# Kernel optimization log

Measured on AMD Instinct MI355X. Metric: run time of the kernel, lower is better.

## Reference

```python
import jax, jax.numpy as jnp
import numpy as np

BS, T = 128, 256
N_AGENTS, STATE_DIM, EMBED_DIM, HYPERNET_EMBED = 32, 512, 64, 256


def setup_inputs() -> dict:
    key = jax.random.key(0)
    ks = jax.random.split(key, 16)
    s = 0.02  # param init scale
    return {
        "agent_qs": jax.random.normal(ks[0], (BS, T, N_AGENTS), jnp.float32),
        "states": jax.random.normal(ks[1], (BS, T, STATE_DIM), jnp.float32),
        "w1_0": jax.random.normal(ks[2], (HYPERNET_EMBED, STATE_DIM), jnp.float32) * s,
        "b1_0": jax.random.normal(ks[3], (HYPERNET_EMBED,), jnp.float32) * s,
        "w1_2": jax.random.normal(ks[4], (EMBED_DIM * N_AGENTS, HYPERNET_EMBED), jnp.float32) * s,
        "b1_2": jax.random.normal(ks[5], (EMBED_DIM * N_AGENTS,), jnp.float32) * s,
        "wf_0": jax.random.normal(ks[6], (HYPERNET_EMBED, STATE_DIM), jnp.float32) * s,
        "bf_0": jax.random.normal(ks[7], (HYPERNET_EMBED,), jnp.float32) * s,
        "wf_2": jax.random.normal(ks[8], (EMBED_DIM, HYPERNET_EMBED), jnp.float32) * s,
        "bf_2": jax.random.normal(ks[9], (EMBED_DIM,), jnp.float32) * s,
        "hb_w": jax.random.normal(ks[10], (EMBED_DIM, STATE_DIM), jnp.float32) * s,
        "hb_b": jax.random.normal(ks[11], (EMBED_DIM,), jnp.float32) * s,
        "v0_w": jax.random.normal(ks[12], (EMBED_DIM, STATE_DIM), jnp.float32) * s,
        "v0_b": jax.random.normal(ks[13], (EMBED_DIM,), jnp.float32) * s,
        "v2_w": jax.random.normal(ks[14], (1, EMBED_DIM), jnp.float32) * s,
        "v2_b": jax.random.normal(ks[15], (1,), jnp.float32) * s,
    }


def reference(agent_qs, states, w1_0, b1_0, w1_2, b1_2, wf_0, bf_0, wf_2, bf_2,
              hb_w, hb_b, v0_w, v0_b, v2_w, v2_b):
    bs = agent_qs.shape[0]
    s = states.reshape(-1, STATE_DIM)          # [B, S]
    q = agent_qs.reshape(-1, 1, N_AGENTS)       # [B, 1, A]
    # hypernet-generated first-layer weights (positive via abs)
    h1 = jax.nn.relu(s @ w1_0.T + b1_0)
    w1 = jnp.abs(h1 @ w1_2.T + b1_2).reshape(-1, N_AGENTS, EMBED_DIM)  # [B, A, E]
    b1 = (s @ hb_w.T + hb_b).reshape(-1, 1, EMBED_DIM)                 # [B, 1, E]
    hidden = jax.nn.elu(jnp.einsum('bia,bae->bie', q, w1) + b1)        # [B, 1, E]
    # hypernet-generated final weights
    hf = jax.nn.relu(s @ wf_0.T + bf_0)
    w_final = jnp.abs(hf @ wf_2.T + bf_2).reshape(-1, EMBED_DIM, 1)    # [B, E, 1]
    v = (jax.nn.relu(s @ v0_w.T + v0_b) @ v2_w.T + v2_b).reshape(-1, 1, 1)
    y = jnp.einsum('bie,beo->bio', hidden, w_final) + v                # [B, 1, 1]
    return y.reshape(bs, -1, 1)
```

## Files before the change

kernel.cpp:

```cpp
#include <hip/hip_runtime.h>


#define SDIM 512
#define HD   256
#define EDIM 64
#define NAG  32

typedef short short8v __attribute__((ext_vector_type(8)));
typedef short short4v __attribute__((ext_vector_type(4)));
typedef float f32x4  __attribute__((ext_vector_type(4)));

__device__ __forceinline__ unsigned short f2bf(float f) {
  unsigned int u = __float_as_uint(f);
  unsigned int r = (u + 0x7FFFu + ((u >> 16) & 1u)) >> 16;
  return (unsigned short)r;
}

__device__ __forceinline__ short4v cvt4(float4 a) {
  short4v r;
  r[0] = (short)f2bf(a.x); r[1] = (short)f2bf(a.y);
  r[2] = (short)f2bf(a.z); r[3] = (short)f2bf(a.w);
  return r;
}

__global__ void qmix_convert(const float* __restrict__ w1_0, const float* __restrict__ wf_0,
                             const float* __restrict__ hb_w, const float* __restrict__ v0_w,
                             const float* __restrict__ w1_2, const float* __restrict__ wf_2,
                             unsigned short* __restrict__ W0cat, unsigned short* __restrict__ w12b,
                             unsigned short* __restrict__ wf2b) {
  int i = blockIdx.x * 256 + threadIdx.x;
  if (i < 327680) {
    float v;
    if (i < 131072)      v = w1_0[i];
    else if (i < 262144) v = wf_0[i - 131072];
    else if (i < 294912) v = hb_w[i - 262144];
    else                 v = v0_w[i - 294912];
    W0cat[i] = f2bf(v);
  } else if (i < 851968) {
    w12b[i - 327680] = f2bf(w1_2[i - 327680]);
  } else if (i < 868352) {
    wf2b[i - 851968] = f2bf(wf_2[i - 851968]);
  }
}

__global__ __launch_bounds__(512, 2) void qmix_main(
    const float* __restrict__ agent_qs, const float* __restrict__ states,
    const unsigned short* __restrict__ W0cat, const unsigned short* __restrict__ w12b,
    const unsigned short* __restrict__ wf2b,
    const float* __restrict__ b1_0, const float* __restrict__ bf_0,
    const float* __restrict__ hb_b, const float* __restrict__ v0_b,
    const float* __restrict__ v2_w, const float* __restrict__ b1_2,
    const float* __restrict__ bf_2, const float* __restrict__ v2_b,
    float* __restrict__ out)
{
  __shared__ unsigned short sA[64 * 512];
  __shared__ unsigned short bb[2][16384];
  __shared__ float b1t[64 * 65];
  __shared__ float q_lds[64 * 33];
  __shared__ float vrow[64];
  __shared__ float ypart[2][64];

  const int t    = threadIdx.x;
  const int r0   = blockIdx.x * 64;
  const int wave = t >> 6, lane = t & 63;
  const int lrow = lane & 15, lk = lane >> 4;

  const float4* gS4 = (const float4*)(states + (size_t)r0 * SDIM);
  float4 L[16];
#pragma unroll
  for (int it = 0; it < 16; it++) L[it] = gS4[it * 512 + t];
  float4 qreg = ((const float4*)(agent_qs + (size_t)r0 * NAG))[t];

  const int colbase = wave * 80;
  const unsigned short* bp[5];
#pragma unroll
  for (int f = 0; f < 5; f++)
    bp[f] = W0cat + (size_t)(colbase + f * 16 + lrow) * SDIM + 8 * lk;
  short8v bregs[2][5];
#pragma unroll
  for (int f = 0; f < 5; f++) bregs[0][f] = *(const short8v*)(bp[f]);
#pragma unroll
  for (int f = 0; f < 5; f++) bregs[1][f] = *(const short8v*)(bp[f] + 32);

#pragma unroll
  for (int it = 0; it < 16; it++) {
    int idx = it * 512 + t;
    int row = idx >> 7, c4 = idx & 127;
    int byte = (row * 1024 + c4 * 8) ^ ((row & 7) << 4);
    *(short4v*)((char*)sA + byte) = cvt4(L[it]);
  }
  {
    int qrow = t >> 3, qc = (t & 7) * 4;
    q_lds[qrow * 33 + qc + 0] = qreg.x;
    q_lds[qrow * 33 + qc + 1] = qreg.y;
    q_lds[qrow * 33 + qc + 2] = qreg.z;
    q_lds[qrow * 33 + qc + 3] = qreg.w;
  }
  __syncthreads();

  f32x4 acc[4][5];
#pragma unroll
  for (int i = 0; i < 4; i++)
#pragma unroll
    for (int f = 0; f < 5; f++) acc[i][f] = (f32x4){0.f, 0.f, 0.f, 0.f};

#pragma unroll
  for (int ks = 0; ks < 16; ks++) {
    const int p = ks & 1;
    short8v af[4];
#pragma unroll
    for (int i = 0; i < 4; i++) {
      int row = i * 16 + lrow;
      int byte = (row * 1024 + ks * 64 + lk * 16) ^ ((row & 7) << 4);
      af[i] = *(const short8v*)((const char*)sA + byte);
    }
#pragma unroll
    for (int f = 0; f < 5; f++)
#pragma unroll
      for (int i = 0; i < 4; i++)
        acc[i][f] = __builtin_amdgcn_mfma_f32_16x16x32_bf16(af[i], bregs[p][f], acc[i][f], 0, 0, 0);
    if (ks < 14) {
#pragma unroll
      for (int f = 0; f < 5; f++) bregs[p][f] = *(const short8v*)(bp[f] + (ks + 2) * 32);
    }
  }

  __syncthreads();

  {
    float vs[4][4];
#pragma unroll
    for (int i = 0; i < 4; i++)
#pragma unroll
      for (int rr = 0; rr < 4; rr++) vs[i][rr] = 0.f;

#pragma unroll
    for (int f = 0; f < 5; f++) {
      int cb  = colbase + f * 16;
      int col = cb + lrow;
      if (cb < 512) {
        float bv = (cb < 256) ? b1_0[col] : bf_0[col - 256];
#pragma unroll
        for (int i = 0; i < 4; i++)
#pragma unroll
          for (int rr = 0; rr < 4; rr++) {
            int row = i * 16 + lk * 4 + rr;
            float v = fmaxf(acc[i][f][rr] + bv, 0.f);
            int byte = (row * 1024 + col * 2) ^ ((row & 7) << 4);
            *(unsigned short*)((char*)sA + byte) = f2bf(v);
          }
      } else if (cb < 576) {
        int e = col - 512;
        float bv = hb_b[e];
#pragma unroll
        for (int i = 0; i < 4; i++)
#pragma unroll
          for (int rr = 0; rr < 4; rr++) {
            int row = i * 16 + lk * 4 + rr;
            b1t[row * 65 + e] = acc[i][f][rr] + bv;
          }
      } else {
        int e = col - 576;
        float bv = v0_b[e], wv = v2_w[e];
#pragma unroll
        for (int i = 0; i < 4; i++)
#pragma unroll
          for (int rr = 0; rr < 4; rr++)
            vs[i][rr] = fmaf(fmaxf(acc[i][f][rr] + bv, 0.f), wv, vs[i][rr]);
      }
    }
    if (colbase == 560) {
#pragma unroll
      for (int i = 0; i < 4; i++)
#pragma unroll
        for (int rr = 0; rr < 4; rr++) {
          float v = vs[i][rr];
#pragma unroll
          for (int m = 1; m < 16; m <<= 1) v += __shfl_xor(v, m, 64);
          if (lrow == 0) vrow[i * 16 + lk * 4 + rr] = v;
        }
    }
  }

  short8v sreg[4];
#pragma unroll
  for (int rd = 0; rd < 4; rd++)
    sreg[rd] = *(const short8v*)(w12b + rd * 4096 + t * 8);

  __syncthreads();

  const int wr = wave >> 1;
  const int wc = wave & 1;

  short8v afr[8];
  {
    int row = wr * 16 + lrow;
#pragma unroll
    for (int kf = 0; kf < 8; kf++) {
      int byte = (row * 1024 + kf * 64 + lk * 16) ^ ((row & 7) << 4);
      afr[kf] = *(const short8v*)((const char*)sA + byte);
    }
  }

#pragma unroll
  for (int rd = 0; rd < 4; rd++) {
    int Lo = rd * 8192 + t * 16;
    int byte = Lo ^ (((Lo >> 9) & 7) << 4);
    *(short8v*)((char*)bb + byte) = sreg[rd];
  }
  __syncthreads();

  f32x4 hac[2];
  hac[0] = (f32x4){0.f, 0.f, 0.f, 0.f};
  hac[1] = (f32x4){0.f, 0.f, 0.f, 0.f};

#pragma unroll 1
  for (int a = 0; a < NAG; a++) {
    if (a < NAG - 1) {
      const unsigned short* src = w12b + (size_t)(a + 1) * 16384;
#pragma unroll
      for (int rd = 0; rd < 4; rd++)
        sreg[rd] = *(const short8v*)(src + rd * 4096 + t * 8);
    }
    const char* rbase = (const char*)bb + (a & 1) * 32768;

    f32x4 T[2];
    T[0] = (f32x4){0.f, 0.f, 0.f, 0.f};
    T[1] = (f32x4){0.f, 0.f, 0.f, 0.f};
#pragma unroll
    for (int kf = 0; kf < 8; kf++) {
      short8v bfv[2];
#pragma unroll
      for (int j = 0; j < 2; j++) {
        int e = wc * 32 + j * 16 + lrow;
        int Lo = e * 512 + kf * 64 + lk * 16;
        bfv[j] = *(const short8v*)(rbase + (Lo ^ ((e & 7) << 4)));
      }
#pragma unroll
      for (int j = 0; j < 2; j++)
        T[j] = __builtin_amdgcn_mfma_f32_16x16x32_bf16(afr[kf], bfv[j], T[j], 0, 0, 0);
    }

    float bbias[2];
#pragma unroll
    for (int j = 0; j < 2; j++) bbias[j] = b1_2[a * 64 + wc * 32 + j * 16 + lrow];
    float qv[4];
#pragma unroll
    for (int r = 0; r < 4; r++)
      qv[r] = q_lds[(wr * 16 + lk * 4 + r) * 33 + a];
#pragma unroll
    for (int j = 0; j < 2; j++)
#pragma unroll
      for (int r = 0; r < 4; r++)
        hac[j][r] = fmaf(qv[r], fabsf(T[j][r] + bbias[j]), hac[j][r]);

    if (a < NAG - 1) {
      char* wbase = (char*)bb + ((a & 1) ^ 1) * 32768;
#pragma unroll
      for (int rd = 0; rd < 4; rd++) {
        int Lo = rd * 8192 + t * 16;
        *(short8v*)(wbase + (Lo ^ (((Lo >> 9) & 7) << 4))) = sreg[rd];
      }
    }
    __syncthreads();
  }

  f32x4 wfa[2];
  wfa[0] = (f32x4){0.f, 0.f, 0.f, 0.f};
  wfa[1] = (f32x4){0.f, 0.f, 0.f, 0.f};
  {
    int row = wr * 16 + lrow;
#pragma unroll
    for (int kf = 0; kf < 8; kf++) {
      int byte = (row * 1024 + 512 + kf * 64 + lk * 16) ^ ((row & 7) << 4);
      short8v af2 = *(const short8v*)((const char*)sA + byte);
      short8v bf2v[2];
#pragma unroll
      for (int j = 0; j < 2; j++) {
        int e = wc * 32 + j * 16 + lrow;
        bf2v[j] = *(const short8v*)(wf2b + (size_t)e * HD + kf * 32 + 8 * lk);
      }
#pragma unroll
      for (int j = 0; j < 2; j++)
        wfa[j] = __builtin_amdgcn_mfma_f32_16x16x32_bf16(af2, bf2v[j], wfa[j], 0, 0, 0);
    }
  }

  {
    float ys[4];
#pragma unroll
    for (int r = 0; r < 4; r++) ys[r] = 0.f;
#pragma unroll
    for (int r = 0; r < 4; r++) {
      int row = wr * 16 + lk * 4 + r;
#pragma unroll
      for (int j = 0; j < 2; j++) {
        int e = wc * 32 + j * 16 + lrow;
        float pre = hac[j][r] + b1t[row * 65 + e];
        float h = pre > 0.f ? pre : expm1f(pre);
        float wfv = fabsf(wfa[j][r] + bf_2[e]);
        ys[r] = fmaf(h, wfv, ys[r]);
      }
    }
#pragma unroll
    for (int m = 1; m < 16; m <<= 1)
#pragma unroll
      for (int r = 0; r < 4; r++) ys[r] += __shfl_xor(ys[r], m, 64);
    if (lrow == 0) {
#pragma unroll
      for (int r = 0; r < 4; r++)
        ypart[wc][wr * 16 + lk * 4 + r] = ys[r];
    }
  }
  __syncthreads();
  if (t < 64) {
    out[r0 + t] = ypart[0][t] + ypart[1][t] + vrow[t] + v2_b[0];
  }
}

extern "C" void kernel_launch(void* const* d_in, const int* in_sizes, int n_in,
                              void* d_out, int out_size, void* d_ws, size_t ws_size,
                              hipStream_t stream) {
  const float* agent_qs = (const float*)d_in[0];
  const float* states   = (const float*)d_in[1];
  const float* w1_0 = (const float*)d_in[2];
  const float* b1_0 = (const float*)d_in[3];
  const float* w1_2 = (const float*)d_in[4];
  const float* b1_2 = (const float*)d_in[5];
  const float* wf_0 = (const float*)d_in[6];
  const float* bf_0 = (const float*)d_in[7];
  const float* wf_2 = (const float*)d_in[8];
  const float* bf_2 = (const float*)d_in[9];
  const float* hb_w = (const float*)d_in[10];
  const float* hb_b = (const float*)d_in[11];
  const float* v0_w = (const float*)d_in[12];
  const float* v0_b = (const float*)d_in[13];
  const float* v2_w = (const float*)d_in[14];
  const float* v2_b = (const float*)d_in[15];

  char* ws = (char*)d_ws;
  unsigned short* W0cat = (unsigned short*)ws;
  unsigned short* w12b  = (unsigned short*)(ws + 655360);
  unsigned short* wf2b  = (unsigned short*)(ws + 1703936);

  qmix_convert<<<3392, 256, 0, stream>>>(w1_0, wf_0, hb_w, v0_w, w1_2, wf_2,
                                         W0cat, w12b, wf2b);
  qmix_main<<<512, 512, 0, stream>>>(agent_qs, states, W0cat, w12b, wf2b,
                                     b1_0, bf_0, hb_b, v0_b, v2_w, b1_2, bf_2, v2_b,
                                     (float*)d_out);
}
```

Before: 124.8 us.

## Split agent loop across wave groups, load w1_2 fragments directly into registers

The 32-agent hypernet loop no longer stages w1_2 tiles through double-buffered LDS with a block-wide barrier per agent. Instead the waves split into two groups of 16 agents each. Each wave loads its B fragments straight from global memory into registers, software-pipelined across the two 16-column halves, and reuses them across two 16-row A tiles. Partial hidden sums from the two groups are reduced through a new padded LDS buffer, and the final-weight stage is re-tiled over four column groups. This removes 32 barriers and the LDS round trip, but each wave now reads weights from global/L2 more redundantly and holds more registers.

After: 179.4 us. 1.44x slower.

```diff
diff --git a/kernel.cpp b/kernel.cpp
--- a/kernel.cpp
+++ b/kernel.cpp
@@ -54,11 +54,11 @@
     float* __restrict__ out)
 {
   __shared__ unsigned short sA[64 * 512];
-  __shared__ unsigned short bb[2][16384];
+  __shared__ float pbuf[2][64 * 65];
   __shared__ float b1t[64 * 65];
   __shared__ float q_lds[64 * 33];
   __shared__ float vrow[64];
-  __shared__ float ypart[2][64];
+  __shared__ float ypart[4][64];
 
   const int t    = threadIdx.x;
   const int r0   = blockIdx.x * 64;
@@ -182,139 +182,153 @@
     }
   }
 
-  short8v sreg[4];
-#pragma unroll
-  for (int rd = 0; rd < 4; rd++)
-    sreg[rd] = *(const short8v*)(w12b + rd * 4096 + t * 8);
-
-  __syncthreads();
-
-  const int wr = wave >> 1;
+  const int wr = wave >> 2;
+  const int g  = (wave >> 1) & 1;
   const int wc = wave & 1;
 
-  short8v afr[8];
+  short8v bdA[8], bdB[8];
   {
-    int row = wr * 16 + lrow;
+    const unsigned short* src = w12b + ((size_t)((g * 16) * EDIM + wc * 32 + lrow)) * HD + 8 * lk;
+#pragma unroll
+    for (int kf = 0; kf < 8; kf++) bdA[kf] = *(const short8v*)(src + kf * 32);
+  }
+
+  __syncthreads();
+
+  short8v afr[2][8];
+#pragma unroll
+  for (int i = 0; i < 2; i++) {
+    int row = wr * 32 + i * 16 + lrow;
 #pragma unroll
     for (int kf = 0; kf < 8; kf++) {
       int byte = (row * 1024 + kf * 64 + lk * 16) ^ ((row & 7) << 4);
-      afr[kf] = *(const short8v*)((const char*)sA + byte);
-    }
-  }
-
-#pragma unroll
-  for (int rd = 0; rd < 4; rd++) {
-    int Lo = rd * 8192 + t * 16;
-    int byte = Lo ^ (((Lo >> 9) & 7) << 4);
-    *(short8v*)((char*)bb + byte) = sreg[rd];
-  }
-  __syncthreads();
-
-  f32x4 hac[2];
-  hac[0] = (f32x4){0.f, 0.f, 0.f, 0.f};
-  hac[1] = (f32x4){0.f, 0.f, 0.f, 0.f};
+      afr[i][kf] = *(const short8v*)((const char*)sA + byte);
+    }
+  }
+
+  f32x4 hac[2][2];
+#pragma unroll
+  for (int i = 0; i < 2; i++)
+#pragma unroll
+    for (int jb = 0; jb < 2; jb++) hac[i][jb] = (f32x4){0.f, 0.f, 0.f, 0.f};
 
 #pragma unroll 1
-  for (int a = 0; a < NAG; a++) {
-    if (a < NAG - 1) {
-      const unsigned short* src = w12b + (size_t)(a + 1) * 16384;
-#pragma unroll
-      for (int rd = 0; rd < 4; rd++)
-        sreg[rd] = *(const short8v*)(src + rd * 4096 + t * 8);
-    }
-    const char* rbase = (const char*)bb + (a & 1) * 32768;
-
-    f32x4 T[2];
-    T[0] = (f32x4){0.f, 0.f, 0.f, 0.f};
-    T[1] = (f32x4){0.f, 0.f, 0.f, 0.f};
-#pragma unroll
-    for (int kf = 0; kf < 8; kf++) {
-      short8v bfv[2];
-#pragma unroll
-      for (int j = 0; j < 2; j++) {
-        int e = wc * 32 + j * 16 + lrow;
-        int Lo = e * 512 + kf * 64 + lk * 16;
-        bfv[j] = *(const short8v*)(rbase + (Lo ^ ((e & 7) << 4)));
+  for (int s2 = 0; s2 < 16; s2++) {
+    const int a = g * 16 + s2;
+
+    {
+      const unsigned short* src = w12b + ((size_t)(a * EDIM + wc * 32 + 16 + lrow)) * HD + 8 * lk;
+#pragma unroll
+      for (int kf = 0; kf < 8; kf++) bdB[kf] = *(const short8v*)(src + kf * 32);
+    }
+    {
+      f32x4 T[2];
+      T[0] = (f32x4){0.f, 0.f, 0.f, 0.f};
+      T[1] = (f32x4){0.f, 0.f, 0.f, 0.f};
+#pragma unroll
+      for (int kf = 0; kf < 8; kf++)
+#pragma unroll
+        for (int i = 0; i < 2; i++)
+          T[i] = __builtin_amdgcn_mfma_f32_16x16x32_bf16(afr[i][kf], bdA[kf], T[i], 0, 0, 0);
+      float bbias = b1_2[a * EDIM + wc * 32 + lrow];
+#pragma unroll
+      for (int i = 0; i < 2; i++)
+#pragma unroll
+        for (int r = 0; r < 4; r++) {
+          float qv = q_lds[(wr * 32 + i * 16 + lk * 4 + r) * 33 + a];
+          hac[i][0][r] = fmaf(qv, fabsf(T[i][r] + bbias), hac[i][0][r]);
+        }
+    }
+    if (s2 < 15) {
+      const unsigned short* src = w12b + ((size_t)((a + 1) * EDIM + wc * 32 + lrow)) * HD + 8 * lk;
+#pragma unroll
+      for (int kf = 0; kf < 8; kf++) bdA[kf] = *(const short8v*)(src + kf * 32);
+    }
+    {
+      f32x4 T[2];
+      T[0] = (f32x4){0.f, 0.f, 0.f, 0.f};
+      T[1] = (f32x4){0.f, 0.f, 0.f, 0.f};
+#pragma unroll
+      for (int kf = 0; kf < 8; kf++)
+#pragma unroll
+        for (int i = 0; i < 2; i++)
+          T[i] = __builtin_amdgcn_mfma_f32_16x16x32_bf16(afr[i][kf], bdB[kf], T[i], 0, 0, 0);
+      float bbias = b1_2[a * EDIM + wc * 32 + 16 + lrow];
+#pragma unroll
+      for (int i = 0; i < 2; i++)
+#pragma unroll
+        for (int r = 0; r < 4; r++) {
+          float qv = q_lds[(wr * 32 + i * 16 + lk * 4 + r) * 33 + a];
+          hac[i][1][r] = fmaf(qv, fabsf(T[i][r] + bbias), hac[i][1][r]);
+        }
+    }
+  }
+
+#pragma unroll
+  for (int i = 0; i < 2; i++)
+#pragma unroll
+    for (int jb = 0; jb < 2; jb++)
+#pragma unroll
+      for (int r = 0; r < 4; r++) {
+        int row = wr * 32 + i * 16 + lk * 4 + r;
+        int e   = wc * 32 + jb * 16 + lrow;
+        pbuf[g][row * 65 + e] = hac[i][jb][r];
       }
-#pragma unroll
-      for (int j = 0; j < 2; j++)
-        T[j] = __builtin_amdgcn_mfma_f32_16x16x32_bf16(afr[kf], bfv[j], T[j], 0, 0, 0);
-    }
-
-    float bbias[2];
-#pragma unroll
-    for (int j = 0; j < 2; j++) bbias[j] = b1_2[a * 64 + wc * 32 + j * 16 + lrow];
-    float qv[4];
-#pragma unroll
-    for (int r = 0; r < 4; r++)
-      qv[r] = q_lds[(wr * 16 + lk * 4 + r) * 33 + a];
-#pragma unroll
-    for (int j = 0; j < 2; j++)
-#pragma unroll
-      for (int r = 0; r < 4; r++)
-        hac[j][r] = fmaf(qv[r], fabsf(T[j][r] + bbias[j]), hac[j][r]);
-
-    if (a < NAG - 1) {
-      char* wbase = (char*)bb + ((a & 1) ^ 1) * 32768;
-#pragma unroll
-      for (int rd = 0; rd < 4; rd++) {
-        int Lo = rd * 8192 + t * 16;
-        *(short8v*)(wbase + (Lo ^ (((Lo >> 9) & 7) << 4))) = sreg[rd];
-      }
-    }
-    __syncthreads();
-  }
+
+  const int eq = wave & 3;
+  short8v bwf[8];
+#pragma unroll
+  for (int kf = 0; kf < 8; kf++)
+    bwf[kf] = *(const short8v*)(wf2b + (size_t)(eq * 16 + lrow) * HD + kf * 32 + 8 * lk);
+
+  __syncthreads();
 
   f32x4 wfa[2];
   wfa[0] = (f32x4){0.f, 0.f, 0.f, 0.f};
   wfa[1] = (f32x4){0.f, 0.f, 0.f, 0.f};
-  {
-    int row = wr * 16 + lrow;
+#pragma unroll
+  for (int i = 0; i < 2; i++) {
+    int row = wr * 32 + i * 16 + lrow;
 #pragma unroll
     for (int kf = 0; kf < 8; kf++) {
       int byte = (row * 1024 + 512 + kf * 64 + lk * 16) ^ ((row & 7) << 4);
       short8v af2 = *(const short8v*)((const char*)sA + byte);
-      short8v bf2v[2];
-#pragma unroll
-      for (int j = 0; j < 2; j++) {
-        int e = wc * 32 + j * 16 + lrow;
-        bf2v[j] = *(const short8v*)(wf2b + (size_t)e * HD + kf * 32 + 8 * lk);
+      wfa[i] = __builtin_amdgcn_mfma_f32_16x16x32_bf16(af2, bwf[kf], wfa[i], 0, 0, 0);
+    }
+  }
+
+  {
+    float ys[2][4];
+#pragma unroll
+    for (int i = 0; i < 2; i++)
+#pragma unroll
+      for (int r = 0; r < 4; r++) {
+        int row = wr * 32 + i * 16 + lk * 4 + r;
+        int e   = eq * 16 + lrow;
+        float hid = pbuf[0][row * 65 + e] + pbuf[1][row * 65 + e];
+        float pre = hid + b1t[row * 65 + e];
+        float h = pre > 0.f ? pre : expm1f(pre);
+        float wfv = fabsf(wfa[i][r] + bf_2[e]);
+        ys[i][r] = h * wfv;
       }
 #pragma unroll
-      for (int j = 0; j < 2; j++)
-        wfa[j] = __builtin_amdgcn_mfma_f32_16x16x32_bf16(af2, bf2v[j], wfa[j], 0, 0, 0);
-    }
-  }
-
-  {
-    float ys[4];
-#pragma unroll
-    for (int r = 0; r < 4; r++) ys[r] = 0.f;
-#pragma unroll
-    for (int r = 0; r < 4; r++) {
-      int row = wr * 16 + lk * 4 + r;
-#pragma unroll
-      for (int j = 0; j < 2; j++) {
-        int e = wc * 32 + j * 16 + lrow;
-        float pre = hac[j][r] + b1t[row * 65 + e];
-        float h = pre > 0.f ? pre : expm1f(pre);
-        float wfv = fabsf(wfa[j][r] + bf_2[e]);
-        ys[r] = fmaf(h, wfv, ys[r]);
-      }
-    }
-#pragma unroll
     for (int m = 1; m < 16; m <<= 1)
 #pragma unroll
-      for (int r = 0; r < 4; r++) ys[r] += __shfl_xor(ys[r], m, 64);
+      for (int i = 0; i < 2; i++)
+#pragma unroll
+        for (int r = 0; r < 4; r++) ys[i][r] += __shfl_xor(ys[i][r], m, 64);
     if (lrow == 0) {
 #pragma unroll
-      for (int r = 0; r < 4; r++)
-        ypart[wc][wr * 16 + lk * 4 + r] = ys[r];
+      for (int i = 0; i < 2; i++)
+#pragma unroll
+        for (int r = 0; r < 4; r++)
+          ypart[eq][wr * 32 + i * 16 + lk * 4 + r] = ys[i][r];
     }
   }
   __syncthreads();
   if (t < 64) {
-    out[r0 + t] = ypart[0][t] + ypart[1][t] + vrow[t] + v2_b[0];
+    out[r0 + t] = ypart[0][t] + ypart[1][t] + ypart[2][t] + ypart[3][t]
+                + vrow[t] + v2_b[0];
   }
 }
 
```
